# Optimization experiments

Measured on AMD Instinct MI355X. Metric: run time of the kernel, lower is better.

## Reference

```python
import jax, jax.numpy as jnp
import numpy as np

ATT = 512  # attention_size

def setup_inputs() -> dict:
    key = jax.random.key(0)
    k0, k1, k2, k3, k4 = jax.random.split(key, 5)
    B, Sq, Sk, Din, Dmem = 32, 1024, 1024, 512, 512
    inputs = jax.random.normal(k0, (B, Sq, Din), dtype=jnp.float32)
    memory = jax.random.normal(k1, (B, Sk, Dmem), dtype=jnp.float32)
    memory_mask = jax.random.randint(k2, (B, Sk), 0, 2).astype(jnp.int32)
    W_input = (jax.random.normal(k3, (Din, ATT), dtype=jnp.float32) * 0.02)
    W_memory = (jax.random.normal(k4, (Dmem, ATT), dtype=jnp.float32) * 0.02)
    return {"inputs": inputs, "memory": memory, "memory_mask": memory_mask,
            "W_input": W_input, "W_memory": W_memory}

def reference(inputs, memory, memory_mask, W_input, W_memory):
    # projections (bias=False) + ReLU; dropout=0 -> identity
    x = jax.nn.relu(jnp.einsum('bqd,da->bqa', inputs, W_input))   # [B,Sq,A]
    m = jax.nn.relu(jnp.einsum('bkd,da->bka', memory, W_memory))  # [B,Sk,A]
    scale = 1.0 / jnp.sqrt(jnp.asarray(ATT, dtype=inputs.dtype))
    logits = jnp.einsum('bqa,bka->bqk', x, m) * scale             # [B,Sq,Sk]
    mask = (memory_mask[:, None, :] != 0)                         # [B,1,Sk] broadcast over Sq
    logits = jnp.where(mask, logits, jnp.asarray(-1e30, dtype=logits.dtype))
    score = jax.nn.softmax(logits, axis=-1)
    context = jnp.einsum('bqk,bkd->bqd', score, memory)           # [B,Sq,Dmem]
    return jnp.concatenate([context, inputs], axis=-1)            # [B,Sq,Dmem+Din]
```

## Files before the change

### kernel.cpp

```cpp
#include <hip/hip_runtime.h>

typedef __bf16 bf16x8 __attribute__((ext_vector_type(8)));
typedef float f32x4 __attribute__((ext_vector_type(4)));

__device__ __forceinline__ unsigned short f2bf(float f) {
    union { float f; unsigned u; } v; v.f = f;
    unsigned r = v.u + 0x7FFFu + ((v.u >> 16) & 1u);
    return (unsigned short)(r >> 16);
}

__global__ __launch_bounds__(256) void mask_scan_kernel(
    const int* __restrict__ mask, int* __restrict__ kidx,
    int* __restrict__ cnt, int* __restrict__ padded)
{
    const int b = blockIdx.x;
    const int* m = mask + b * 1024;
    const int t = threadIdx.x;
    int v[4]; int s = 0;
#pragma unroll
    for (int e = 0; e < 4; e++) { v[e] = (m[t * 4 + e] != 0) ? 1 : 0; s += v[e]; }
    const int lane = t & 63, wv = t >> 6;
    int x = s;
#pragma unroll
    for (int off = 1; off < 64; off <<= 1) {
        int y = __shfl_up(x, off, 64);
        if (lane >= off) x += y;
    }
    __shared__ int wsum[4];
    if (lane == 63) wsum[wv] = x;
    __syncthreads();
    int base = 0;
    for (int w = 0; w < wv; w++) base += wsum[w];
    int pos = base + x - s;
#pragma unroll
    for (int e = 0; e < 4; e++)
        if (v[e]) kidx[b * 1024 + pos++] = t * 4 + e;
    if (t == 255) {
        int total = base + x;
        cnt[b] = total;
        padded[b] = (total + 127) & ~127;
    }
}

__global__ __launch_bounds__(256) void transpose_w_kernel(
    const float* __restrict__ W0, const float* __restrict__ W1,
    unsigned short* __restrict__ D0, unsigned short* __restrict__ D1)
{
    __shared__ float tile[32][33];
    const float* src = blockIdx.z ? W1 : W0;
    unsigned short* dst = blockIdx.z ? D1 : D0;
    const int s0 = blockIdx.x * 32, d0 = blockIdx.y * 32;
    const int t = threadIdx.x, tr = t >> 5, tc = t & 31;
#pragma unroll
    for (int i = 0; i < 4; i++)
        tile[tr + i * 8][tc] = src[(size_t)(s0 + tr + i * 8) * 512 + d0 + tc];
    __syncthreads();
#pragma unroll
    for (int i = 0; i < 4; i++)
        dst[(size_t)(d0 + tr + i * 8) * 512 + s0 + tc] = f2bf(tile[tc][tr + i * 8]);
}

__global__ __launch_bounds__(256) void gather_mem_kernel(
    const float* __restrict__ memory, const int* __restrict__ kidx,
    const int* __restrict__ cnt, const int* __restrict__ padded,
    unsigned short* __restrict__ MemG, unsigned short* __restrict__ MemGT)
{
    const int b = blockIdx.z;
    const int j0 = blockIdx.x * 32, d0 = blockIdx.y * 32;
    if (j0 >= padded[b]) return;
    const int nb = cnt[b];
    __shared__ float tile[32][33];
    const float* src = memory + (size_t)b * 1024 * 512;
    const int t = threadIdx.x, tr = t >> 5, tc = t & 31;
#pragma unroll
    for (int i = 0; i < 4; i++) {
        int j = j0 + tr + i * 8;
        float v = 0.f;
        if (j < nb) v = src[(size_t)kidx[b * 1024 + j] * 512 + d0 + tc];
        tile[tr + i * 8][tc] = v;
        MemG[(size_t)b * 1024 * 512 + (size_t)j * 512 + d0 + tc] = f2bf(v);
    }
    __syncthreads();
#pragma unroll
    for (int i = 0; i < 4; i++) {
        int d = d0 + tr + i * 8;
        MemGT[(size_t)b * 512 * 1024 + (size_t)d * 1024 + j0 + tc] = f2bf(tile[tc][tr + i * 8]);
    }
}

__global__ __launch_bounds__(256) void fuse_inputs_kernel(
    const float4* __restrict__ in, uint2* __restrict__ in_bf16, float4* __restrict__ out)
{
    int i = blockIdx.x * 256 + threadIdx.x;
    int bq = i >> 7;
    int d  = i & 127;
    float4 v = in[i];
    out[(size_t)bq * 256 + 128 + d] = v;
    union { unsigned short u[4]; uint2 p; } pk;
    pk.u[0] = f2bf(v.x); pk.u[1] = f2bf(v.y);
    pk.u[2] = f2bf(v.z); pk.u[3] = f2bf(v.w);
    in_bf16[i] = pk.p;
}

template<int CMODE, int LIMA, int LIMB, int KDYN>
__global__ __launch_bounds__(256, 2) void gemm_bt(
    const unsigned short* __restrict__ A, const unsigned short* __restrict__ Bt,
    void* __restrict__ Cptr, int K, int lda, int ldb, float scale,
    const int* __restrict__ cnt, const int* __restrict__ padded,
    float* __restrict__ rowsum,
    long long aStride, long long bStride, long long cStride, int ldc)
{
    const int z = blockIdx.z;
    const int rowA = blockIdx.y * 128;
    const int rowB = blockIdx.x * 128;
    if (LIMA && rowA >= padded[z]) return;
    if (LIMB && rowB >= padded[z]) return;
    const int Kz = KDYN ? padded[z] : K;

    __shared__ __align__(16) unsigned short As[128 * 32];
    __shared__ __align__(16) unsigned short Bs[128 * 32];

    const int t = threadIdx.x;
    const int lane = t & 63;
    const int wave = t >> 6;

    const unsigned short* Ab = A + (size_t)z * aStride;
    const unsigned short* Bb = Bt + (size_t)z * bStride;

    f32x4 acc[4][4];
#pragma unroll
    for (int i = 0; i < 4; i++)
#pragma unroll
        for (int j = 0; j < 4; j++) acc[i][j] = f32x4{0.f, 0.f, 0.f, 0.f};

    const int wm = (wave >> 1) * 64;
    const int wn = (wave & 1) * 64;
    const int lrow = lane & 15;
    const int lk = (lane >> 4) * 8;

    const int sr = lane >> 2;
    const int skk = (lane & 3) * 8;
    const int c0 = wave, c1 = wave + 4;

    for (int kt = 0; kt < Kz; kt += 32) {
        const unsigned short* gb0 = Bb + (size_t)(rowB + c0 * 16 + sr) * ldb + kt + skk;
        const unsigned short* gb1 = Bb + (size_t)(rowB + c1 * 16 + sr) * ldb + kt + skk;
        __builtin_amdgcn_global_load_lds((const __attribute__((address_space(1))) void*)gb0,
                                         (__attribute__((address_space(3))) void*)&Bs[c0 * 512], 16, 0, 0);
        __builtin_amdgcn_global_load_lds((const __attribute__((address_space(1))) void*)gb1,
                                         (__attribute__((address_space(3))) void*)&Bs[c1 * 512], 16, 0, 0);
        const unsigned short* ga0 = Ab + (size_t)(rowA + c0 * 16 + sr) * lda + kt + skk;
        const unsigned short* ga1 = Ab + (size_t)(rowA + c1 * 16 + sr) * lda + kt + skk;
        __builtin_amdgcn_global_load_lds((const __attribute__((address_space(1))) void*)ga0,
                                         (__attribute__((address_space(3))) void*)&As[c0 * 512], 16, 0, 0);
        __builtin_amdgcn_global_load_lds((const __attribute__((address_space(1))) void*)ga1,
                                         (__attribute__((address_space(3))) void*)&As[c1 * 512], 16, 0, 0);
        __syncthreads();

        bf16x8 a[4], b[4];
#pragma unroll
        for (int i = 0; i < 4; i++) a[i] = *(const bf16x8*)&As[(wm + i * 16 + lrow) * 32 + lk];
#pragma unroll
        for (int j = 0; j < 4; j++) b[j] = *(const bf16x8*)&Bs[(wn + j * 16 + lrow) * 32 + lk];
#pragma unroll
        for (int i = 0; i < 4; i++)
#pragma unroll
            for (int j = 0; j < 4; j++)
                acc[i][j] = __builtin_amdgcn_mfma_f32_16x16x32_bf16(a[i], b[j], acc[i][j], 0, 0, 0);
        __syncthreads();
    }

    const int orow = (lane >> 4) * 4;
    const int ocol = lane & 15;

    if constexpr (CMODE == 0) {
        unsigned short* C = (unsigned short*)Cptr + (size_t)z * cStride;
#pragma unroll
        for (int i = 0; i < 4; i++)
#pragma unroll
            for (int j = 0; j < 4; j++) {
                int col = rowB + wn + j * 16 + ocol;
#pragma unroll
                for (int r = 0; r < 4; r++) {
                    int rw = rowA + wm + i * 16 + orow + r;
                    C[(size_t)rw * ldc + col] = f2bf(fmaxf(acc[i][j][r], 0.f));
                }
            }
    } else if constexpr (CMODE == 1) {
        unsigned short* C = (unsigned short*)Cptr + (size_t)z * cStride;
        const int nb = cnt[z];
        float* rs = rowsum + (size_t)z * 1024;
#pragma unroll
        for (int i = 0; i < 4; i++) {
            float part[4] = {0.f, 0.f, 0.f, 0.f};
#pragma unroll
            for (int j = 0; j < 4; j++) {
                int col = rowB + wn + j * 16 + ocol;
#pragma unroll
                for (int r = 0; r < 4; r++) {
                    float p = (col < nb) ? __expf(acc[i][j][r] * scale) : 0.f;
                    part[r] += p;
                    int rw = rowA + wm + i * 16 + orow + r;
                    C[(size_t)rw * ldc + col] = f2bf(p);
                }
            }
#pragma unroll
            for (int r = 0; r < 4; r++) {
                float s = part[r];
                s += __shfl_xor(s, 1, 64);
                s += __shfl_xor(s, 2, 64);
                s += __shfl_xor(s, 4, 64);
                s += __shfl_xor(s, 8, 64);
                if (ocol == 0) atomicAdd(&rs[rowA + wm + i * 16 + orow + r], s);
            }
        }
    } else {
        float* C = (float*)Cptr + (size_t)z * cStride;
        const float* rs = rowsum + (size_t)z * 1024;
#pragma unroll
        for (int i = 0; i < 4; i++) {
            float inv[4];
#pragma unroll
            for (int r = 0; r < 4; r++)
                inv[r] = 1.0f / rs[rowA + wm + i * 16 + orow + r];
#pragma unroll
            for (int j = 0; j < 4; j++) {
                int col = rowB + wn + j * 16 + ocol;
#pragma unroll
                for (int r = 0; r < 4; r++) {
                    int rw = rowA + wm + i * 16 + orow + r;
                    C[(size_t)rw * ldc + col] = acc[i][j][r] * inv[r];
                }
            }
        }
    }
}

extern "C" void kernel_launch(void* const* d_in, const int* in_sizes, int n_in,
                              void* d_out, int out_size, void* d_ws, size_t ws_size,
                              hipStream_t stream)
{
    const float* inputs = (const float*)d_in[0];
    const float* memory = (const float*)d_in[1];
    const int*   mmask  = (const int*)d_in[2];
    const float* W_in   = (const float*)d_in[3];
    const float* W_mem  = (const float*)d_in[4];
    float* out = (float*)d_out;

    char* ws = (char*)d_ws;
    const unsigned long long MB = 1048576ull;
    unsigned short* Wt_in  = (unsigned short*)(ws);
    unsigned short* Wt_mem = (unsigned short*)(ws + 524288);
    unsigned short* InB16  = (unsigned short*)(ws + 1 * MB);
    unsigned short* MemG   = (unsigned short*)(ws + 33 * MB);
    unsigned short* P      = (unsigned short*)(ws + 1 * MB);
    unsigned short* MemGT  = (unsigned short*)(ws + 65 * MB);
    unsigned short* Xq     = (unsigned short*)(ws + 97 * MB);
    unsigned short* Xm     = (unsigned short*)(ws + 129 * MB);
    float*          rowsum = (float*)(ws + 161 * MB);
    int*            kidx   = (int*)(ws + 161 * MB + 131072);
    int*            cntp   = (int*)(ws + 161 * MB + 262144);
    int*            padp   = (int*)(ws + 161 * MB + 262144 + 128);

    const float scale = 0.04419417382415922f;

    mask_scan_kernel<<<32, 256, 0, stream>>>(mmask, kidx, cntp, padp);
    transpose_w_kernel<<<dim3(16, 16, 2), 256, 0, stream>>>(W_in, W_mem, Wt_in, Wt_mem);

    gather_mem_kernel<<<dim3(32, 16, 32), 256, 0, stream>>>(
        memory, kidx, cntp, padp, MemG, MemGT);

    fuse_inputs_kernel<<<16384, 256, 0, stream>>>(
        (const float4*)inputs, (uint2*)InB16, (float4*)out);

    hipMemsetAsync(rowsum, 0, 32 * 1024 * sizeof(float), stream);

    gemm_bt<0, 0, 0, 0><<<dim3(4, 256, 1), 256, 0, stream>>>(
        InB16, Wt_in, Xq, 512, 512, 512, 0.f, nullptr, nullptr, nullptr,
        0, 0, 0, 512);
    gemm_bt<0, 1, 0, 0><<<dim3(4, 8, 32), 256, 0, stream>>>(
        MemG, Wt_mem, Xm, 512, 512, 512, 0.f, nullptr, padp, nullptr,
        1024ll * 512, 0, 1024ll * 512, 512);

    gemm_bt<1, 0, 1, 0><<<dim3(8, 8, 32), 256, 0, stream>>>(
        Xq, Xm, P, 512, 512, 512, scale, cntp, padp, rowsum,
        1024ll * 512, 1024ll * 512, 1024ll * 1024, 1024);

    gemm_bt<2, 0, 0, 1><<<dim3(4, 8, 32), 256, 0, stream>>>(
        P, MemGT, out, 1024, 1024, 1024, 1.f, nullptr, padp, rowsum,
        1024ll * 1024, 512ll * 1024, 1024ll * 1024, 1024);
}
```

Measured before the change: 437.9 us.

## Rewrite GEMM as 256x256 tile, 8-wave kernel with double-buffered swizzled LDS prefetch

Replaces the 128x128 single-buffered GEMM with a 256x256 tile kernel using 512 threads, a 64-deep K step and 128KB of double-buffered LDS. Global-to-LDS loads for the next K tile are interleaved with MFMA phases and guarded by explicit barriers and waitcnt, with s_setprio raised around the MFMA blocks. An XOR swizzle on the LDS layout is meant to avoid bank conflicts. The larger tile raises data reuse and hides load latency, but it coarsens padded-row skipping, uses far more registers and LDS per block, and leaves fewer blocks to spread across CUs.

Result: faster. 420.6 us (-3.9%).

```diff
diff --git a/kernel.cpp b/kernel.cpp
--- a/kernel.cpp
+++ b/kernel.cpp
@@ -103,7 +103,7 @@
 }
 
 template<int CMODE, int LIMA, int LIMB, int KDYN>
-__global__ __launch_bounds__(256, 2) void gemm_bt(
+__global__ __launch_bounds__(512, 2) void gemm256(
     const unsigned short* __restrict__ A, const unsigned short* __restrict__ Bt,
     void* __restrict__ Cptr, int K, int lda, int ldb, float scale,
     const int* __restrict__ cnt, const int* __restrict__ padded,
@@ -111,79 +111,150 @@
     long long aStride, long long bStride, long long cStride, int ldc)
 {
     const int z = blockIdx.z;
-    const int rowA = blockIdx.y * 128;
-    const int rowB = blockIdx.x * 128;
+    const int rowA = blockIdx.y * 256;
+    const int rowB = blockIdx.x * 256;
     if (LIMA && rowA >= padded[z]) return;
     if (LIMB && rowB >= padded[z]) return;
     const int Kz = KDYN ? padded[z] : K;
-
-    __shared__ __align__(16) unsigned short As[128 * 32];
-    __shared__ __align__(16) unsigned short Bs[128 * 32];
+    const int nt = Kz >> 6;
+
+    __shared__ __align__(16) unsigned char lds[131072];
 
     const int t = threadIdx.x;
+    const int w = t >> 6;
     const int lane = t & 63;
-    const int wave = t >> 6;
+    const int wm = w >> 2;
+    const int wn = w & 3;
+    const int l15 = lane & 15;
+    const int sx = (((lane >> 4) ^ ((l15 >> 1) & 3)) << 4);
 
     const unsigned short* Ab = A + (size_t)z * aStride;
     const unsigned short* Bb = Bt + (size_t)z * bStride;
 
-    f32x4 acc[4][4];
-#pragma unroll
-    for (int i = 0; i < 4; i++)
+    const int r0 = t >> 2;
+    const int sl = (t & 3) ^ ((t >> 3) & 3);
+    const unsigned short* aS0 = Ab + (size_t)(rowA + r0) * lda + sl * 8;
+    const unsigned short* aS1 = aS0 + (size_t)128 * lda;
+    const unsigned short* bS0 = Bb + (size_t)(rowB + r0) * ldb + sl * 8;
+    const unsigned short* bS1 = bS0 + (size_t)128 * ldb;
+
+    const int wofs = w * 1024;
+    const int aRd = (wm * 128 + l15) * 64 + sx;
+    const int bRd = 32768 + (wn * 64 + l15) * 64 + sx;
+
+    f32x4 acc[8][4];
+#pragma unroll
+    for (int i = 0; i < 8; i++)
 #pragma unroll
         for (int j = 0; j < 4; j++) acc[i][j] = f32x4{0.f, 0.f, 0.f, 0.f};
 
-    const int wm = (wave >> 1) * 64;
-    const int wn = (wave & 1) * 64;
-    const int lrow = lane & 15;
-    const int lk = (lane >> 4) * 8;
-
-    const int sr = lane >> 2;
-    const int skk = (lane & 3) * 8;
-    const int c0 = wave, c1 = wave + 4;
-
-    for (int kt = 0; kt < Kz; kt += 32) {
-        const unsigned short* gb0 = Bb + (size_t)(rowB + c0 * 16 + sr) * ldb + kt + skk;
-        const unsigned short* gb1 = Bb + (size_t)(rowB + c1 * 16 + sr) * ldb + kt + skk;
-        __builtin_amdgcn_global_load_lds((const __attribute__((address_space(1))) void*)gb0,
-                                         (__attribute__((address_space(3))) void*)&Bs[c0 * 512], 16, 0, 0);
-        __builtin_amdgcn_global_load_lds((const __attribute__((address_space(1))) void*)gb1,
-                                         (__attribute__((address_space(3))) void*)&Bs[c1 * 512], 16, 0, 0);
-        const unsigned short* ga0 = Ab + (size_t)(rowA + c0 * 16 + sr) * lda + kt + skk;
-        const unsigned short* ga1 = Ab + (size_t)(rowA + c1 * 16 + sr) * lda + kt + skk;
-        __builtin_amdgcn_global_load_lds((const __attribute__((address_space(1))) void*)ga0,
-                                         (__attribute__((address_space(3))) void*)&As[c0 * 512], 16, 0, 0);
-        __builtin_amdgcn_global_load_lds((const __attribute__((address_space(1))) void*)ga1,
-                                         (__attribute__((address_space(3))) void*)&As[c1 * 512], 16, 0, 0);
-        __syncthreads();
-
-        bf16x8 a[4], b[4];
-#pragma unroll
-        for (int i = 0; i < 4; i++) a[i] = *(const bf16x8*)&As[(wm + i * 16 + lrow) * 32 + lk];
-#pragma unroll
-        for (int j = 0; j < 4; j++) b[j] = *(const bf16x8*)&Bs[(wn + j * 16 + lrow) * 32 + lk];
+#define GLL(SRC, DOFS) __builtin_amdgcn_global_load_lds(                        \
+        (const __attribute__((address_space(1))) void*)(SRC),                   \
+        (__attribute__((address_space(3))) void*)&lds[DOFS], 16, 0, 0)
+#define STAGEA(BUF, KH, KEL) do {                                               \
+        GLL(aS0 + (KEL), (BUF) * 65536 + (KH) * 16384 + wofs);                  \
+        GLL(aS1 + (KEL), (BUF) * 65536 + (KH) * 16384 + wofs + 8192); } while (0)
+#define STAGEB(BUF, KH, KEL) do {                                               \
+        GLL(bS0 + (KEL), (BUF) * 65536 + 32768 + (KH) * 16384 + wofs);          \
+        GLL(bS1 + (KEL), (BUF) * 65536 + 32768 + (KH) * 16384 + wofs + 8192); } while (0)
+
+    STAGEA(0, 0, 0); STAGEB(0, 0, 0); STAGEA(0, 1, 32); STAGEB(0, 1, 32);
+    asm volatile("s_waitcnt vmcnt(4)" ::: "memory");
+    __builtin_amdgcn_s_barrier();
+
+    for (int tt = 0; tt < nt; ++tt) {
+        const int cur = (tt & 1) * 65536;
+        const int nxt = (tt & 1) ^ 1;
+        const bool pf = (tt + 1) < nt;
+        const int kn = (tt + 1) * 64;
+        bf16x8 af[4], bf0[4], bf1[4];
+
+#pragma unroll
+        for (int i = 0; i < 4; i++) af[i]  = *(const bf16x8*)&lds[cur + aRd + i * 1024];
+#pragma unroll
+        for (int j = 0; j < 4; j++) bf0[j] = *(const bf16x8*)&lds[cur + bRd + j * 1024];
+        if (pf) STAGEA(nxt, 0, kn);
+        __builtin_amdgcn_s_barrier();
+        asm volatile("s_waitcnt lgkmcnt(0)" ::: "memory");
+        __builtin_amdgcn_sched_barrier(0);
+        __builtin_amdgcn_s_setprio(1);
 #pragma unroll
         for (int i = 0; i < 4; i++)
 #pragma unroll
             for (int j = 0; j < 4; j++)
-                acc[i][j] = __builtin_amdgcn_mfma_f32_16x16x32_bf16(a[i], b[j], acc[i][j], 0, 0, 0);
-        __syncthreads();
-    }
+                acc[i][j] = __builtin_amdgcn_mfma_f32_16x16x32_bf16(af[i], bf0[j], acc[i][j], 0, 0, 0);
+        __builtin_amdgcn_s_setprio(0);
+        __builtin_amdgcn_s_barrier();
+
+#pragma unroll
+        for (int i = 0; i < 4; i++) af[i] = *(const bf16x8*)&lds[cur + aRd + (i + 4) * 1024];
+        if (pf) STAGEB(nxt, 0, kn);
+        __builtin_amdgcn_s_barrier();
+        asm volatile("s_waitcnt lgkmcnt(0)" ::: "memory");
+        __builtin_amdgcn_sched_barrier(0);
+        __builtin_amdgcn_s_setprio(1);
+#pragma unroll
+        for (int i = 0; i < 4; i++)
+#pragma unroll
+            for (int j = 0; j < 4; j++)
+                acc[i + 4][j] = __builtin_amdgcn_mfma_f32_16x16x32_bf16(af[i], bf0[j], acc[i + 4][j], 0, 0, 0);
+        __builtin_amdgcn_s_setprio(0);
+        if (pf) { asm volatile("s_waitcnt vmcnt(4)" ::: "memory"); }
+        else    { asm volatile("s_waitcnt vmcnt(0)" ::: "memory"); }
+        __builtin_amdgcn_s_barrier();
+
+#pragma unroll
+        for (int i = 0; i < 4; i++) af[i]  = *(const bf16x8*)&lds[cur + 16384 + aRd + i * 1024];
+#pragma unroll
+        for (int j = 0; j < 4; j++) bf1[j] = *(const bf16x8*)&lds[cur + 16384 + bRd + j * 1024];
+        if (pf) STAGEA(nxt, 1, kn + 32);
+        __builtin_amdgcn_s_barrier();
+        asm volatile("s_waitcnt lgkmcnt(0)" ::: "memory");
+        __builtin_amdgcn_sched_barrier(0);
+        __builtin_amdgcn_s_setprio(1);
+#pragma unroll
+        for (int i = 0; i < 4; i++)
+#pragma unroll
+            for (int j = 0; j < 4; j++)
+                acc[i][j] = __builtin_amdgcn_mfma_f32_16x16x32_bf16(af[i], bf1[j], acc[i][j], 0, 0, 0);
+        __builtin_amdgcn_s_setprio(0);
+        __builtin_amdgcn_s_barrier();
+
+#pragma unroll
+        for (int i = 0; i < 4; i++) af[i] = *(const bf16x8*)&lds[cur + 16384 + aRd + (i + 4) * 1024];
+        if (pf) STAGEB(nxt, 1, kn + 32);
+        __builtin_amdgcn_s_barrier();
+        asm volatile("s_waitcnt lgkmcnt(0)" ::: "memory");
+        __builtin_amdgcn_sched_barrier(0);
+        __builtin_amdgcn_s_setprio(1);
+#pragma unroll
+        for (int i = 0; i < 4; i++)
+#pragma unroll
+            for (int j = 0; j < 4; j++)
+                acc[i + 4][j] = __builtin_amdgcn_mfma_f32_16x16x32_bf16(af[i], bf1[j], acc[i + 4][j], 0, 0, 0);
+        __builtin_amdgcn_s_setprio(0);
+        if (pf) { asm volatile("s_waitcnt vmcnt(4)" ::: "memory"); }
+        __builtin_amdgcn_s_barrier();
+    }
+
+#undef GLL
+#undef STAGEA
+#undef STAGEB
 
     const int orow = (lane >> 4) * 4;
-    const int ocol = lane & 15;
+    const int ocol = l15;
 
     if constexpr (CMODE == 0) {
         unsigned short* C = (unsigned short*)Cptr + (size_t)z * cStride;
 #pragma unroll
-        for (int i = 0; i < 4; i++)
-#pragma unroll
-            for (int j = 0; j < 4; j++) {
-                int col = rowB + wn + j * 16 + ocol;
+        for (int mf = 0; mf < 8; mf++)
+#pragma unroll
+            for (int nf = 0; nf < 4; nf++) {
+                const int col = rowB + wn * 64 + nf * 16 + ocol;
 #pragma unroll
                 for (int r = 0; r < 4; r++) {
-                    int rw = rowA + wm + i * 16 + orow + r;
-                    C[(size_t)rw * ldc + col] = f2bf(fmaxf(acc[i][j][r], 0.f));
+                    const int rw = rowA + wm * 128 + mf * 16 + orow + r;
+                    C[(size_t)rw * ldc + col] = f2bf(fmaxf(acc[mf][nf][r], 0.f));
                 }
             }
     } else if constexpr (CMODE == 1) {
@@ -191,16 +262,16 @@
         const int nb = cnt[z];
         float* rs = rowsum + (size_t)z * 1024;
 #pragma unroll
-        for (int i = 0; i < 4; i++) {
+        for (int mf = 0; mf < 8; mf++) {
             float part[4] = {0.f, 0.f, 0.f, 0.f};
 #pragma unroll
-            for (int j = 0; j < 4; j++) {
-                int col = rowB + wn + j * 16 + ocol;
+            for (int nf = 0; nf < 4; nf++) {
+                const int col = rowB + wn * 64 + nf * 16 + ocol;
 #pragma unroll
                 for (int r = 0; r < 4; r++) {
-                    float p = (col < nb) ? __expf(acc[i][j][r] * scale) : 0.f;
+                    float p = (col < nb) ? __expf(acc[mf][nf][r] * scale) : 0.f;
                     part[r] += p;
-                    int rw = rowA + wm + i * 16 + orow + r;
+                    const int rw = rowA + wm * 128 + mf * 16 + orow + r;
                     C[(size_t)rw * ldc + col] = f2bf(p);
                 }
             }
@@ -211,25 +282,26 @@
                 s += __shfl_xor(s, 2, 64);
                 s += __shfl_xor(s, 4, 64);
                 s += __shfl_xor(s, 8, 64);
-                if (ocol == 0) atomicAdd(&rs[rowA + wm + i * 16 + orow + r], s);
+                if (ocol == 0)
+                    atomicAdd(&rs[rowA + wm * 128 + mf * 16 + orow + r], s);
             }
         }
     } else {
         float* C = (float*)Cptr + (size_t)z * cStride;
         const float* rs = rowsum + (size_t)z * 1024;
 #pragma unroll
-        for (int i = 0; i < 4; i++) {
+        for (int mf = 0; mf < 8; mf++) {
             float inv[4];
 #pragma unroll
             for (int r = 0; r < 4; r++)
-                inv[r] = 1.0f / rs[rowA + wm + i * 16 + orow + r];
-#pragma unroll
-            for (int j = 0; j < 4; j++) {
-                int col = rowB + wn + j * 16 + ocol;
+                inv[r] = 1.0f / rs[rowA + wm * 128 + mf * 16 + orow + r];
+#pragma unroll
+            for (int nf = 0; nf < 4; nf++) {
+                const int col = rowB + wn * 64 + nf * 16 + ocol;
 #pragma unroll
                 for (int r = 0; r < 4; r++) {
-                    int rw = rowA + wm + i * 16 + orow + r;
-                    C[(size_t)rw * ldc + col] = acc[i][j][r] * inv[r];
+                    const int rw = rowA + wm * 128 + mf * 16 + orow + r;
+                    C[(size_t)rw * ldc + col] = acc[mf][nf][r] * inv[r];
                 }
             }
         }
@@ -275,18 +347,18 @@
 
     hipMemsetAsync(rowsum, 0, 32 * 1024 * sizeof(float), stream);
 
-    gemm_bt<0, 0, 0, 0><<<dim3(4, 256, 1), 256, 0, stream>>>(
+    gemm256<0, 0, 0, 0><<<dim3(2, 128, 1), 512, 0, stream>>>(
         InB16, Wt_in, Xq, 512, 512, 512, 0.f, nullptr, nullptr, nullptr,
         0, 0, 0, 512);
-    gemm_bt<0, 1, 0, 0><<<dim3(4, 8, 32), 256, 0, stream>>>(
+    gemm256<0, 1, 0, 0><<<dim3(2, 4, 32), 512, 0, stream>>>(
         MemG, Wt_mem, Xm, 512, 512, 512, 0.f, nullptr, padp, nullptr,
         1024ll * 512, 0, 1024ll * 512, 512);
 
-    gemm_bt<1, 0, 1, 0><<<dim3(8, 8, 32), 256, 0, stream>>>(
+    gemm256<1, 0, 1, 0><<<dim3(4, 4, 32), 512, 0, stream>>>(
         Xq, Xm, P, 512, 512, 512, scale, cntp, padp, rowsum,
         1024ll * 512, 1024ll * 512, 1024ll * 1024, 1024);
 
-    gemm_bt<2, 0, 0, 1><<<dim3(4, 8, 32), 256, 0, stream>>>(
+    gemm256<2, 0, 0, 1><<<dim3(2, 4, 32), 512, 0, stream>>>(
         P, MemGT, out, 1024, 1024, 1024, 1.f, nullptr, padp, rowsum,
         1024ll * 1024, 512ll * 1024, 1024ll * 1024, 1024);
 }
```
